# Kernel optimization log

Measured on AMD Instinct MI355X. Metric: run time of the kernel, lower is better.

The kernel has to match this reference:

```python
import jax, jax.numpy as jnp
import numpy as np

PERIOD = 4
B, T, D = 8, 8192, 512


def setup_inputs() -> dict:
    key = jax.random.key(0)
    x = jax.random.normal(key, (B, T, D), dtype=jnp.float32)
    # original draws mask_idx ~ Uniform{0..period-1}; fixed here for determinism
    return {"x": x, "mask_idx": 2}


def reference(x, mask_idx):
    # Equivalent math to the TF layer: the block-diagonal [P, D, P*D] filter +
    # stride-P conv1d + reshape simply zeros timestep `mask_idx` inside every
    # consecutive frame of `PERIOD` timesteps. (With T % PERIOD == 0, TF 'SAME'
    # padding is zero, so the equivalence is exact.)
    b, t, d = x.shape
    xr = x.reshape(b, t // PERIOD, PERIOD, d)            # [B, T/P, P, D]
    keep = (jnp.arange(PERIOD) != mask_idx).astype(x.dtype)  # [P]
    out = xr * keep[None, None, :, None]
    return out.reshape(b, t, d)
```

## Files before the change

kernel.cpp:

```cpp
#include <hip/hip_runtime.h>


#define PERIOD 4

typedef float f32x4 __attribute__((ext_vector_type(4)));

__global__ __launch_bounds__(256)
void pd_mask_fast(const f32x4* __restrict__ x,
                  const int* __restrict__ mask_p,
                  f32x4* __restrict__ out) {
    constexpr int STRIDE = 2048 * 256;
    const int tid = blockIdx.x * 256 + threadIdx.x;
    const int m = *mask_p;
    if (((tid >> 7) & (PERIOD - 1)) == m) {
        const f32x4 zero = (f32x4){0.f, 0.f, 0.f, 0.f};
        #pragma unroll
        for (int k = 0; k < 16; ++k)
            out[tid + k * STRIDE] = zero;
    } else {
        #pragma unroll
        for (int r = 0; r < 2; ++r) {
            f32x4 v[8];
            #pragma unroll
            for (int k = 0; k < 8; ++k)
                v[k] = x[tid + (r * 8 + k) * STRIDE];
            #pragma unroll
            for (int k = 0; k < 8; ++k)
                out[tid + (r * 8 + k) * STRIDE] = v[k];
        }
    }
}

__global__ __launch_bounds__(256)
void pd_mask_generic(const f32x4* __restrict__ x,
                     const int* __restrict__ mask_p,
                     f32x4* __restrict__ out, int n4) {
    const int m = *mask_p;
    const f32x4 zero = (f32x4){0.f, 0.f, 0.f, 0.f};
    const int stride = gridDim.x * blockDim.x;
    for (int i = blockIdx.x * blockDim.x + threadIdx.x; i < n4; i += stride) {
        const int t = i >> 7;
        out[i] = ((t & (PERIOD - 1)) == m) ? zero : x[i];
    }
}

extern "C" void kernel_launch(void* const* d_in, const int* in_sizes, int n_in,
                              void* d_out, int out_size, void* d_ws, size_t ws_size,
                              hipStream_t stream) {
    const f32x4* x      = (const f32x4*)d_in[0];
    const int*   mask_p = (const int*)d_in[1];
    f32x4*       out    = (f32x4*)d_out;

    const int n4 = out_size / 4;
    constexpr int BLOCK = 256, GRID = 2048, ITERS = 16;

    if (n4 == GRID * BLOCK * ITERS) {
        pd_mask_fast<<<GRID, BLOCK, 0, stream>>>(x, mask_p, out);
    } else {
        int grid = (n4 + BLOCK - 1) / BLOCK;
        if (grid > 2048) grid = 2048;
        pd_mask_generic<<<grid, BLOCK, 0, stream>>>(x, mask_p, out, n4);
    }
}
```

Measured before the change: 241.0 us.

## Split masking into full copy kernel plus masked-slice zero-fill kernel

```diff
diff --git a/kernel.cpp b/kernel.cpp
--- a/kernel.cpp
+++ b/kernel.cpp
@@ -6,28 +6,23 @@
 typedef float f32x4 __attribute__((ext_vector_type(4)));
 
 __global__ __launch_bounds__(256)
-void pd_mask_fast(const f32x4* __restrict__ x,
-                  const int* __restrict__ mask_p,
-                  f32x4* __restrict__ out) {
-    constexpr int STRIDE = 2048 * 256;
-    const int tid = blockIdx.x * 256 + threadIdx.x;
+void copy_all(const f32x4* __restrict__ x, f32x4* __restrict__ out, int n4) {
+    const int stride = gridDim.x * blockDim.x;
+    int i = blockIdx.x * blockDim.x + threadIdx.x;
+    #pragma unroll 4
+    for (; i < n4; i += stride)
+        out[i] = x[i];
+}
+
+__global__ __launch_bounds__(256)
+void fill_masked(const int* __restrict__ mask_p, f32x4* __restrict__ out, int nq) {
     const int m = *mask_p;
-    if (((tid >> 7) & (PERIOD - 1)) == m) {
-        const f32x4 zero = (f32x4){0.f, 0.f, 0.f, 0.f};
-        #pragma unroll
-        for (int k = 0; k < 16; ++k)
-            out[tid + k * STRIDE] = zero;
-    } else {
-        #pragma unroll
-        for (int r = 0; r < 2; ++r) {
-            f32x4 v[8];
-            #pragma unroll
-            for (int k = 0; k < 8; ++k)
-                v[k] = x[tid + (r * 8 + k) * STRIDE];
-            #pragma unroll
-            for (int k = 0; k < 8; ++k)
-                out[tid + (r * 8 + k) * STRIDE] = v[k];
-        }
+    const f32x4 zero = (f32x4){0.f, 0.f, 0.f, 0.f};
+    const int stride = gridDim.x * blockDim.x;
+    for (int j = blockIdx.x * blockDim.x + threadIdx.x; j < nq; j += stride) {
+        const int frame = j >> 7;
+        const int off   = j & 127;
+        out[frame * 512 + m * 128 + off] = zero;
     }
 }
 
@@ -52,13 +47,13 @@
     f32x4*       out    = (f32x4*)d_out;
 
     const int n4 = out_size / 4;
-    constexpr int BLOCK = 256, GRID = 2048, ITERS = 16;
-
-    if (n4 == GRID * BLOCK * ITERS) {
-        pd_mask_fast<<<GRID, BLOCK, 0, stream>>>(x, mask_p, out);
+    if ((n4 & 511) == 0) {
+        copy_all<<<2048, 256, 0, stream>>>(x, out, n4);
+        const int nq = n4 / 4;
+        fill_masked<<<1024, 256, 0, stream>>>(mask_p, out, nq);
     } else {
-        int grid = (n4 + BLOCK - 1) / BLOCK;
+        int grid = (n4 + 255) / 256;
         if (grid > 2048) grid = 2048;
-        pd_mask_generic<<<grid, BLOCK, 0, stream>>>(x, mask_p, out, n4);
+        pd_mask_generic<<<grid, 256, 0, stream>>>(x, mask_p, out, n4);
     }
 }
```

New measurement: 247.8 us. 2.8% more time.
